# Performance work log

Measured on AMD Instinct MI355X. Metric: run time of the kernel, lower is better.

The kernel has to match this reference:

```python
import jax, jax.numpy as jnp
import numpy as np

V, E, H, B, S, K, L = 32000, 512, 1024, 16, 128, 15, 1


def setup_inputs() -> dict:
    key = jax.random.key(0)
    ks = jax.random.split(key, 12)
    s = 0.02
    W_emb = jax.random.normal(ks[0], (V, E), jnp.float32) * s
    W_emb = W_emb.at[0].set(0.0)  # padding_idx=0
    return {
        "input_ids": jax.random.randint(ks[1], (B, S), 0, V),
        "hidden": jnp.zeros((L, B, H), jnp.float32),
        "stop_indicators": jax.random.randint(ks[2], (B, S), 0, 2),
        "W_emb": W_emb,
        "W_ih": jax.random.normal(ks[3], (H, E), jnp.float32) * s,
        "b_ih": jax.random.normal(ks[4], (H,), jnp.float32) * s,
        "W_hh": jax.random.normal(ks[5], (H, H), jnp.float32) * s,
        "b_hh": jax.random.normal(ks[6], (H,), jnp.float32) * s,
        "W_dec": jax.random.normal(ks[7], (V, H), jnp.float32) * s,
        "b_dec": jax.random.normal(ks[8], (V,), jnp.float32) * s,
        "beta": jax.random.uniform(ks[9], (K, V), jnp.float32),
        "theta": jax.random.uniform(ks[10], (K,), jnp.float32),
    }


def reference(input_ids, hidden, stop_indicators, W_emb, W_ih, b_ih, W_hh, b_hh,
              W_dec, b_dec, beta, theta):
    # Embedding lookup: [B, S, E]
    emb = W_emb[input_ids]
    xs = jnp.swapaxes(emb, 0, 1)  # [S, B, E] time-major for scan
    h0 = hidden[0]                # [B, H]

    # Elman RNN (tanh), single layer, batch_first semantics
    def step(h, x):
        h_new = jnp.tanh(x @ W_ih.T + b_ih + h @ W_hh.T + b_hh)
        return h_new, h_new

    hT, outs = jax.lax.scan(step, h0, xs)      # outs: [S, B, H]
    output = jnp.swapaxes(outs, 0, 1)          # [B, S, H]

    decoded = output @ W_dec.T + b_dec         # [B, S, V]

    # Topic additions: single fused GEMV theta @ beta (replaces per-vocab loop)
    topic_additions = theta @ beta             # [V]
    stop_mask = (stop_indicators == 0).astype(decoded.dtype)[..., None]  # [B,S,1]
    decoded = decoded + topic_additions * stop_mask

    return decoded, hT[None]  # hidden back as [layers=1, B, H]
```

## Files before the change

kernel.cpp:

```cpp
#include <hip/hip_runtime.h>
#include <stdint.h>

#define V_ 32000
#define E_ 512
#define H_ 1024
#define B_ 16
#define S_ 128
#define K_ 15

typedef float floatx4 __attribute__((ext_vector_type(4)));
typedef short shortx8 __attribute__((ext_vector_type(8)));
typedef __bf16 bf16x8 __attribute__((ext_vector_type(8)));

static __device__ __forceinline__ unsigned short f2b(float f) {
  union { float f; uint32_t u; } v; v.f = f;
  uint32_t u = v.u;
  u += 0x7FFFu + ((u >> 16) & 1u);
  return (unsigned short)(u >> 16);
}

static __device__ __forceinline__ shortx8 cvt8(floatx4 a, floatx4 b) {
  shortx8 r;
  r[0] = (short)f2b(a[0]); r[1] = (short)f2b(a[1]);
  r[2] = (short)f2b(a[2]); r[3] = (short)f2b(a[3]);
  r[4] = (short)f2b(b[0]); r[5] = (short)f2b(b[1]);
  r[6] = (short)f2b(b[2]); r[7] = (short)f2b(b[3]);
  return r;
}

static __device__ __forceinline__ floatx4 mfma_bf16(shortx8 a, shortx8 b, floatx4 c) {
  return __builtin_amdgcn_mfma_f32_16x16x32_bf16(
      __builtin_bit_cast(bf16x8, a), __builtin_bit_cast(bf16x8, b), c, 0, 0, 0);
}


__global__ void k_zero(int* __restrict__ p, int n) {
  int i = blockIdx.x * blockDim.x + threadIdx.x;
  if (i < n) p[i] = 0;
}

__global__ void k_topic(const float* __restrict__ beta, const float* __restrict__ theta,
                        float* __restrict__ topic) {
  int n = blockIdx.x * blockDim.x + threadIdx.x;
  float s = 0.f;
#pragma unroll
  for (int k = 0; k < K_; ++k) s += theta[k] * beta[k * V_ + n];
  topic[n] = s;
}

__global__ void k_cvt(const float* __restrict__ src, unsigned short* __restrict__ dst) {
  size_t i = (size_t)(blockIdx.x * blockDim.x + threadIdx.x) * 8;
  floatx4 f0 = *(const floatx4*)(src + i);
  floatx4 f1 = *(const floatx4*)(src + i + 4);
  *(shortx8*)(dst + i) = cvt8(f0, f1);
}

__global__ __launch_bounds__(256, 2) void k_gemm_pre(
    const int* __restrict__ ids, const float* __restrict__ W_emb,
    const float* __restrict__ W_ih, const float* __restrict__ b_ih,
    const float* __restrict__ b_hh, float* __restrict__ pre) {
  __shared__ unsigned short As[128 * 72];
  __shared__ unsigned short Bs[128 * 72];
  const int tid = threadIdx.x;
  const int gn0 = blockIdx.x * 128;
  const int gm0 = blockIdx.y * 128;
  const int wave = tid >> 6, lane = tid & 63;
  const int wm = (wave >> 1) * 64, wn = (wave & 1) * 64;
  const int lr = lane & 15, lg = lane >> 4;

  floatx4 acc[4][4];
#pragma unroll
  for (int i = 0; i < 4; ++i)
#pragma unroll
    for (int j = 0; j < 4; ++j) acc[i][j] = (floatx4)0.0f;

  for (int k0 = 0; k0 < E_; k0 += 64) {
#pragma unroll
    for (int c = 0; c < 4; ++c) {
      int q = c * 256 + tid;
      int row = q >> 3, kc = (q & 7) * 8;
      int m = gm0 + row;
      int id = ids[(m & 15) * S_ + (m >> 4)];
      const float* ga = W_emb + (size_t)id * E_ + k0 + kc;
      floatx4 a0 = *(const floatx4*)ga;
      floatx4 a1 = *(const floatx4*)(ga + 4);
      *(shortx8*)&As[row * 72 + kc] = cvt8(a0, a1);
      const float* gb = W_ih + (size_t)(gn0 + row) * E_ + k0 + kc;
      floatx4 c0 = *(const floatx4*)gb;
      floatx4 c1 = *(const floatx4*)(gb + 4);
      *(shortx8*)&Bs[row * 72 + kc] = cvt8(c0, c1);
    }
    __syncthreads();
#pragma unroll
    for (int ks = 0; ks < 64; ks += 32) {
      shortx8 af[4], bfr[4];
#pragma unroll
      for (int i = 0; i < 4; ++i)
        af[i] = *(const shortx8*)&As[(wm + i * 16 + lr) * 72 + ks + lg * 8];
#pragma unroll
      for (int j = 0; j < 4; ++j)
        bfr[j] = *(const shortx8*)&Bs[(wn + j * 16 + lr) * 72 + ks + lg * 8];
#pragma unroll
      for (int i = 0; i < 4; ++i)
#pragma unroll
        for (int j = 0; j < 4; ++j) acc[i][j] = mfma_bf16(af[i], bfr[j], acc[i][j]);
    }
    __syncthreads();
  }
#pragma unroll
  for (int i = 0; i < 4; ++i) {
#pragma unroll
    for (int r = 0; r < 4; ++r) {
      int m = gm0 + wm + i * 16 + lg * 4 + r;
#pragma unroll
      for (int j = 0; j < 4; ++j) {
        int n = gn0 + wn + j * 16 + lr;
        pre[(size_t)m * H_ + n] = acc[i][j][r] + b_ih[n] + b_hh[n];
      }
    }
  }
}

__global__ __launch_bounds__(128, 1) void k_rnn(
    const float* __restrict__ hidden0, const float* __restrict__ W_hh,
    const float* __restrict__ pre, unsigned short* __restrict__ hb,
    unsigned short* __restrict__ act,
    float* __restrict__ hT_out,
    int* __restrict__ flags) {
  const int tid = threadIdx.x, bid = blockIdx.x;
  const int lane = tid & 63, wave = tid >> 6;
  const int lr = lane & 15, lg = lane >> 4;
  const int nn = bid * 32 + wave * 16 + lr;

  shortx8 bfr[32];
#pragma unroll
  for (int s = 0; s < 32; ++s) {
    const float* g = W_hh + (size_t)nn * H_ + s * 32 + lg * 8;
    floatx4 f0 = *(const floatx4*)g;
    floatx4 f1 = *(const floatx4*)(g + 4);
    bfr[s] = cvt8(f0, f1);
  }

  {
    int gt = (bid * 128 + tid) * 4;
#pragma unroll
    for (int u = 0; u < 4; ++u) {
      int e = gt + u;
      int b = e >> 10, n = e & 1023;
      hb[(((n >> 5) * 64 + ((n >> 3) & 3) * 16 + b) << 3) + (n & 7)] = f2b(hidden0[e]);
    }
  }

  __builtin_amdgcn_fence(__ATOMIC_RELEASE, "workgroup");
  __syncthreads();
  if (tid == 0)
    __hip_atomic_store(&flags[bid * 32], 1, __ATOMIC_RELEASE, __HIP_MEMORY_SCOPE_AGENT);

  float prer[4], prer2[4];
#pragma unroll
  for (int r = 0; r < 4; ++r) prer[r] = pre[((size_t)(lg * 4 + r)) * H_ + nn];

  if (tid < 32) {
    while (__hip_atomic_load(&flags[tid * 32], __ATOMIC_RELAXED,
                             __HIP_MEMORY_SCOPE_AGENT) < 1)
      __builtin_amdgcn_s_sleep(1);
  }
  __syncthreads();
  __builtin_amdgcn_fence(__ATOMIC_ACQUIRE, "agent");

  const int sft = (((nn >> 5) * 64 + ((nn >> 3) & 3) * 16) << 3) + (nn & 7);

  for (int t = 0; t < S_; ++t) {
    const unsigned short* hcur = hb + (t & 1) * (B_ * H_);
    unsigned short* hnxt = hb + ((t + 1) & 1) * (B_ * H_);

    floatx4 a0 = (floatx4)0.f, a1 = (floatx4)0.f, a2 = (floatx4)0.f, a3 = (floatx4)0.f;
#pragma unroll
    for (int s = 0; s < 32; s += 4) {
      shortx8 f0 = *(const shortx8*)&hcur[((s + 0) * 64 + lane) * 8];
      shortx8 f1 = *(const shortx8*)&hcur[((s + 1) * 64 + lane) * 8];
      shortx8 f2 = *(const shortx8*)&hcur[((s + 2) * 64 + lane) * 8];
      shortx8 f3 = *(const shortx8*)&hcur[((s + 3) * 64 + lane) * 8];
      a0 = mfma_bf16(f0, bfr[s + 0], a0);
      a1 = mfma_bf16(f1, bfr[s + 1], a1);
      a2 = mfma_bf16(f2, bfr[s + 2], a2);
      a3 = mfma_bf16(f3, bfr[s + 3], a3);
    }
    floatx4 acc = (a0 + a1) + (a2 + a3);

#pragma unroll
    for (int r = 0; r < 4; ++r) {
      int b = lg * 4 + r;
      float h = tanhf(acc[r] + prer[r]);
      unsigned short h16 = f2b(h);
      hnxt[sft + b * 8] = h16;
      act[((size_t)b * S_ + t) * H_ + nn] = h16;
      if (t == S_ - 1) hT_out[b * H_ + nn] = h;
    }

    if (t < S_ - 1) {
      __builtin_amdgcn_fence(__ATOMIC_RELEASE, "workgroup");
      __syncthreads();
      if (tid == 0)
        __hip_atomic_store(&flags[bid * 32], t + 2, __ATOMIC_RELEASE,
                           __HIP_MEMORY_SCOPE_AGENT);
#pragma unroll
      for (int r = 0; r < 4; ++r)
        prer2[r] = pre[((size_t)(t + 1) * B_ + lg * 4 + r) * H_ + nn];
      if (tid < 32) {
        while (__hip_atomic_load(&flags[tid * 32], __ATOMIC_RELAXED,
                                 __HIP_MEMORY_SCOPE_AGENT) < t + 2)
          __builtin_amdgcn_s_sleep(1);
      }
      __syncthreads();
      __builtin_amdgcn_fence(__ATOMIC_ACQUIRE, "agent");
#pragma unroll
      for (int r = 0; r < 4; ++r) prer[r] = prer2[r];
    }
  }
}

__global__ __launch_bounds__(256, 2) void k_gemm_dec(
    const unsigned short* __restrict__ A, const unsigned short* __restrict__ Bw,
    const float* __restrict__ b_dec, const float* __restrict__ topic,
    const int* __restrict__ stop, float* __restrict__ out) {
  __shared__ unsigned short As[128 * 72];
  __shared__ unsigned short Bs[128 * 72];
  const int tid = threadIdx.x;
  const int gn0 = blockIdx.x * 128;
  const int gm0 = blockIdx.y * 128;
  const int wave = tid >> 6, lane = tid & 63;
  const int wm = (wave >> 1) * 64, wn = (wave & 1) * 64;
  const int lr = lane & 15, lg = lane >> 4;

  floatx4 acc[4][4];
#pragma unroll
  for (int i = 0; i < 4; ++i)
#pragma unroll
    for (int j = 0; j < 4; ++j) acc[i][j] = (floatx4)0.0f;

  for (int k0 = 0; k0 < H_; k0 += 64) {
#pragma unroll
    for (int c = 0; c < 4; ++c) {
      int q = c * 256 + tid;
      int row = q >> 3, kc = (q & 7) * 8;
      *(shortx8*)&As[row * 72 + kc] =
          *(const shortx8*)(A + (size_t)(gm0 + row) * H_ + k0 + kc);
      *(shortx8*)&Bs[row * 72 + kc] =
          *(const shortx8*)(Bw + (size_t)(gn0 + row) * H_ + k0 + kc);
    }
    __syncthreads();
#pragma unroll
    for (int ks = 0; ks < 64; ks += 32) {
      shortx8 af[4], bfr[4];
#pragma unroll
      for (int i = 0; i < 4; ++i)
        af[i] = *(const shortx8*)&As[(wm + i * 16 + lr) * 72 + ks + lg * 8];
#pragma unroll
      for (int j = 0; j < 4; ++j)
        bfr[j] = *(const shortx8*)&Bs[(wn + j * 16 + lr) * 72 + ks + lg * 8];
#pragma unroll
      for (int i = 0; i < 4; ++i)
#pragma unroll
        for (int j = 0; j < 4; ++j) acc[i][j] = mfma_bf16(af[i], bfr[j], acc[i][j]);
    }
    __syncthreads();
  }
#pragma unroll
  for (int i = 0; i < 4; ++i) {
#pragma unroll
    for (int r = 0; r < 4; ++r) {
      int m = gm0 + wm + i * 16 + lg * 4 + r;
      float msk = (stop[m] == 0) ? 1.f : 0.f;
      size_t base = (size_t)m * V_;
#pragma unroll
      for (int j = 0; j < 4; ++j) {
        int n = gn0 + wn + j * 16 + lr;
        out[base + n] = acc[i][j][r] + b_dec[n] + topic[n] * msk;
      }
    }
  }
}

extern "C" void kernel_launch(void* const* d_in, const int* in_sizes, int n_in,
                              void* d_out, int out_size, void* d_ws, size_t ws_size,
                              hipStream_t stream) {
  (void)in_sizes; (void)n_in; (void)out_size; (void)ws_size;
  const int*   ids    = (const int*)d_in[0];
  const float* hidden = (const float*)d_in[1];
  const int*   stop   = (const int*)d_in[2];
  const float* W_emb  = (const float*)d_in[3];
  const float* W_ih   = (const float*)d_in[4];
  const float* b_ih   = (const float*)d_in[5];
  const float* W_hh   = (const float*)d_in[6];
  const float* b_hh   = (const float*)d_in[7];
  const float* W_dec  = (const float*)d_in[8];
  const float* b_dec  = (const float*)d_in[9];
  const float* beta   = (const float*)d_in[10];
  const float* theta  = (const float*)d_in[11];
  float* out = (float*)d_out;

  char* ws = (char*)d_ws;
  size_t off = 0;
  auto alloc = [&](size_t bytes) -> void* {
    void* p = ws + off;
    off = (off + bytes + 255) & ~(size_t)255;
    return p;
  };
  int* flags = (int*)alloc(16384 * sizeof(int));
  float* topic = (float*)alloc((size_t)V_ * 4);
  float* pre = (float*)alloc((size_t)B_ * S_ * H_ * 4);
  unsigned short* act = (unsigned short*)alloc((size_t)B_ * S_ * H_ * 2);
  unsigned short* hb = (unsigned short*)alloc((size_t)2 * B_ * H_ * 2);
  unsigned short* wdec16 = (unsigned short*)alloc((size_t)V_ * H_ * 2);

  k_zero<<<dim3(32), dim3(512), 0, stream>>>(flags, 16384);
  k_topic<<<dim3(V_ / 256), dim3(256), 0, stream>>>(beta, theta, topic);
  k_cvt<<<dim3((V_ * H_) / (256 * 8)), dim3(256), 0, stream>>>(W_dec, wdec16);
  k_gemm_pre<<<dim3(H_ / 128, (B_ * S_) / 128), dim3(256), 0, stream>>>(
      ids, W_emb, W_ih, b_ih, b_hh, pre);
  k_rnn<<<dim3(32), dim3(128), 0, stream>>>(hidden, W_hh, pre, hb, act,
                                            out + (size_t)B_ * S_ * V_, flags);
  k_gemm_dec<<<dim3(V_ / 128, (B_ * S_) / 128), dim3(256), 0, stream>>>(
      act, wdec16, b_dec, topic, stop, out);
}
```

Before: 1.285 ms.

## Halve RNN grid and replace agent fences with write-through stores and coherent loads

The persistent RNN kernel now runs 16 blocks of 256 threads, each owning 64 hidden units, in place of 32 blocks of 128, so fewer blocks take part in the per-step grid barrier. Agent-scope acquire and release fences are replaced by write-through stores (sc0 sc1) of hidden state and flags, a vmcnt wait, and relaxed agent-scope 64-bit atomic loads of the hidden state. The aim is to cut the per-timestep cross-block synchronisation latency that dominates the 128 serial steps. It relies on hand-written cache-policy assembly for memory ordering, which could be fragile or incorrect if visibility is not guaranteed.

Result: faster. 1.227 ms (-4.5%).

```diff
diff --git a/kernel.cpp b/kernel.cpp
--- a/kernel.cpp
+++ b/kernel.cpp
@@ -31,6 +31,17 @@
 static __device__ __forceinline__ floatx4 mfma_bf16(shortx8 a, shortx8 b, floatx4 c) {
   return __builtin_amdgcn_mfma_f32_16x16x32_bf16(
       __builtin_bit_cast(bf16x8, a), __builtin_bit_cast(bf16x8, b), c, 0, 0, 0);
+}
+
+static __device__ __forceinline__ void st_u16_wt(unsigned short* p, unsigned int v) {
+  asm volatile("global_store_short %0, %1, off sc0 sc1" :: "v"(p), "v"(v) : "memory");
+}
+static __device__ __forceinline__ void st_u32_wt(int* p, int v) {
+  asm volatile("global_store_dword %0, %1, off sc0 sc1" :: "v"(p), "v"(v) : "memory");
+}
+static __device__ __forceinline__ unsigned long long ld_u64_cb(const unsigned short* p) {
+  return __hip_atomic_load((const unsigned long long*)p, __ATOMIC_RELAXED,
+                           __HIP_MEMORY_SCOPE_AGENT);
 }
 
 
@@ -121,7 +132,7 @@
   }
 }
 
-__global__ __launch_bounds__(128, 1) void k_rnn(
+__global__ __launch_bounds__(256, 1) void k_rnn(
     const float* __restrict__ hidden0, const float* __restrict__ W_hh,
     const float* __restrict__ pre, unsigned short* __restrict__ hb,
     unsigned short* __restrict__ act,
@@ -130,7 +141,7 @@
   const int tid = threadIdx.x, bid = blockIdx.x;
   const int lane = tid & 63, wave = tid >> 6;
   const int lr = lane & 15, lg = lane >> 4;
-  const int nn = bid * 32 + wave * 16 + lr;
+  const int nn = bid * 64 + wave * 16 + lr;
 
   shortx8 bfr[32];
 #pragma unroll
@@ -142,31 +153,29 @@
   }
 
   {
-    int gt = (bid * 128 + tid) * 4;
+    int gt = (bid * 256 + tid) * 4;
 #pragma unroll
     for (int u = 0; u < 4; ++u) {
       int e = gt + u;
       int b = e >> 10, n = e & 1023;
-      hb[(((n >> 5) * 64 + ((n >> 3) & 3) * 16 + b) << 3) + (n & 7)] = f2b(hidden0[e]);
-    }
-  }
-
-  __builtin_amdgcn_fence(__ATOMIC_RELEASE, "workgroup");
+      st_u16_wt(&hb[(((n >> 5) * 64 + ((n >> 3) & 3) * 16 + b) << 3) + (n & 7)],
+                (unsigned int)f2b(hidden0[e]));
+    }
+  }
+  asm volatile("s_waitcnt vmcnt(0)" ::: "memory");
   __syncthreads();
-  if (tid == 0)
-    __hip_atomic_store(&flags[bid * 32], 1, __ATOMIC_RELEASE, __HIP_MEMORY_SCOPE_AGENT);
+  if (tid == 0) st_u32_wt(&flags[bid * 32], 1);
 
   float prer[4], prer2[4];
 #pragma unroll
   for (int r = 0; r < 4; ++r) prer[r] = pre[((size_t)(lg * 4 + r)) * H_ + nn];
 
-  if (tid < 32) {
+  if (tid < 16) {
     while (__hip_atomic_load(&flags[tid * 32], __ATOMIC_RELAXED,
                              __HIP_MEMORY_SCOPE_AGENT) < 1)
       __builtin_amdgcn_s_sleep(1);
   }
   __syncthreads();
-  __builtin_amdgcn_fence(__ATOMIC_ACQUIRE, "agent");
 
   const int sft = (((nn >> 5) * 64 + ((nn >> 3) & 3) * 16) << 3) + (nn & 7);
 
@@ -177,14 +186,19 @@
     floatx4 a0 = (floatx4)0.f, a1 = (floatx4)0.f, a2 = (floatx4)0.f, a3 = (floatx4)0.f;
 #pragma unroll
     for (int s = 0; s < 32; s += 4) {
-      shortx8 f0 = *(const shortx8*)&hcur[((s + 0) * 64 + lane) * 8];
-      shortx8 f1 = *(const shortx8*)&hcur[((s + 1) * 64 + lane) * 8];
-      shortx8 f2 = *(const shortx8*)&hcur[((s + 2) * 64 + lane) * 8];
-      shortx8 f3 = *(const shortx8*)&hcur[((s + 3) * 64 + lane) * 8];
-      a0 = mfma_bf16(f0, bfr[s + 0], a0);
-      a1 = mfma_bf16(f1, bfr[s + 1], a1);
-      a2 = mfma_bf16(f2, bfr[s + 2], a2);
-      a3 = mfma_bf16(f3, bfr[s + 3], a3);
+      union { unsigned long long q[2]; shortx8 v; } u0, u1, u2, u3;
+      const unsigned short* p0 = &hcur[((s + 0) * 64 + lane) * 8];
+      const unsigned short* p1 = &hcur[((s + 1) * 64 + lane) * 8];
+      const unsigned short* p2 = &hcur[((s + 2) * 64 + lane) * 8];
+      const unsigned short* p3 = &hcur[((s + 3) * 64 + lane) * 8];
+      u0.q[0] = ld_u64_cb(p0); u0.q[1] = ld_u64_cb(p0 + 4);
+      u1.q[0] = ld_u64_cb(p1); u1.q[1] = ld_u64_cb(p1 + 4);
+      u2.q[0] = ld_u64_cb(p2); u2.q[1] = ld_u64_cb(p2 + 4);
+      u3.q[0] = ld_u64_cb(p3); u3.q[1] = ld_u64_cb(p3 + 4);
+      a0 = mfma_bf16(u0.v, bfr[s + 0], a0);
+      a1 = mfma_bf16(u1.v, bfr[s + 1], a1);
+      a2 = mfma_bf16(u2.v, bfr[s + 2], a2);
+      a3 = mfma_bf16(u3.v, bfr[s + 3], a3);
     }
     floatx4 acc = (a0 + a1) + (a2 + a3);
 
@@ -193,27 +207,24 @@
       int b = lg * 4 + r;
       float h = tanhf(acc[r] + prer[r]);
       unsigned short h16 = f2b(h);
-      hnxt[sft + b * 8] = h16;
+      st_u16_wt(&hnxt[sft + b * 8], (unsigned int)h16);
       act[((size_t)b * S_ + t) * H_ + nn] = h16;
       if (t == S_ - 1) hT_out[b * H_ + nn] = h;
     }
 
     if (t < S_ - 1) {
-      __builtin_amdgcn_fence(__ATOMIC_RELEASE, "workgroup");
+      asm volatile("s_waitcnt vmcnt(0)" ::: "memory");
       __syncthreads();
-      if (tid == 0)
-        __hip_atomic_store(&flags[bid * 32], t + 2, __ATOMIC_RELEASE,
-                           __HIP_MEMORY_SCOPE_AGENT);
+      if (tid == 0) st_u32_wt(&flags[bid * 32], t + 2);
 #pragma unroll
       for (int r = 0; r < 4; ++r)
         prer2[r] = pre[((size_t)(t + 1) * B_ + lg * 4 + r) * H_ + nn];
-      if (tid < 32) {
+      if (tid < 16) {
         while (__hip_atomic_load(&flags[tid * 32], __ATOMIC_RELAXED,
                                  __HIP_MEMORY_SCOPE_AGENT) < t + 2)
           __builtin_amdgcn_s_sleep(1);
       }
       __syncthreads();
-      __builtin_amdgcn_fence(__ATOMIC_ACQUIRE, "agent");
 #pragma unroll
       for (int r = 0; r < 4; ++r) prer[r] = prer2[r];
     }
@@ -319,7 +330,7 @@
   k_cvt<<<dim3((V_ * H_) / (256 * 8)), dim3(256), 0, stream>>>(W_dec, wdec16);
   k_gemm_pre<<<dim3(H_ / 128, (B_ * S_) / 128), dim3(256), 0, stream>>>(
       ids, W_emb, W_ih, b_ih, b_hh, pre);
-  k_rnn<<<dim3(32), dim3(128), 0, stream>>>(hidden, W_hh, pre, hb, act,
+  k_rnn<<<dim3(16), dim3(256), 0, stream>>>(hidden, W_hh, pre, hb, act,
                                             out + (size_t)B_ * S_ * V_, flags);
   k_gemm_dec<<<dim3(V_ / 128, (B_ * S_) / 128), dim3(256), 0, stream>>>(
       act, wdec16, b_dec, topic, stop, out);
```
